# Kernel tuning notes

Hardware: AMD Instinct MI355X
Metric: run time of the kernel (lower is better)

## Reference

```python
import jax, jax.numpy as jnp
import numpy as np

DECAY = 0.99


def setup_inputs() -> dict:
    key = jax.random.key(0)
    k1, k2, k3 = jax.random.split(key, 3)
    B, D, H, W = 16, 128, 32, 32
    K = 8192
    z_e = jax.random.normal(k1, (B, D, H, W), dtype=jnp.float32)
    codebook = jax.random.normal(k2, (K, D), dtype=jnp.float32)
    ema_count = jnp.ones((K,), dtype=jnp.float32)
    ema_weight = codebook  # buffer initialized as codebook.clone()
    return {"z_e": z_e, "codebook": codebook, "ema_count": ema_count, "ema_weight": ema_weight}


def reference(z_e, codebook, ema_count, ema_weight):
    B, D, H, W = z_e.shape
    K = codebook.shape[0]
    # (B,D,H,W) -> (N,D)
    z_flat = z_e.transpose(0, 2, 3, 1).reshape(-1, D)
    # squared L2 distances: ||z||^2 - 2 z.C^T + ||C||^2  -> (N,K)
    dist = (
        jnp.sum(z_flat * z_flat, axis=1, keepdims=True)
        - 2.0 * (z_flat @ codebook.T)
        + jnp.sum(codebook * codebook, axis=1)[None, :]
    )
    indices = jnp.argmin(dist, axis=1)  # (N,)
    z_q = codebook[indices].reshape(B, H, W, D).transpose(0, 3, 1, 2)
    # EMA codebook update (training path, no grad)
    counts = jax.ops.segment_sum(jnp.ones_like(indices, dtype=jnp.float32), indices, num_segments=K)
    dw = jax.ops.segment_sum(z_flat, indices, num_segments=K)  # (K,D)
    new_count = ema_count * DECAY + (1.0 - DECAY) * counts
    new_weight = ema_weight * DECAY + (1.0 - DECAY) * dw
    new_codebook = new_weight / jnp.maximum(new_count, 1.0)[:, None]
    # straight-through estimator
    z_q_st = z_e + jax.lax.stop_gradient(z_q - z_e)
    return (z_q_st, indices.reshape(B, H, W), new_codebook, new_count, new_weight)
```

## Files before the change

### kernel.cpp

```cpp
#include <hip/hip_runtime.h>

#define D 128
#define HW 1024
#define NROWS 16384
#define K 8192
#define NU 16

#define OUT0 0
#define OUT1 2097152
#define OUT2 2113536
#define OUT3 3162112
#define OUT4 3170304

typedef __attribute__((ext_vector_type(8))) _Float16 half8;
typedef __attribute__((ext_vector_type(16))) float f32x16;
typedef unsigned short u16;
typedef unsigned long long u64;

__device__ __forceinline__ void gld16(const u16* gsrc, u16* ldst) {
    __builtin_amdgcn_global_load_lds(
        (const __attribute__((address_space(1))) unsigned int*)gsrc,
        (__attribute__((address_space(3))) unsigned int*)ldst,
        16, 0, 0);
}

__global__ __launch_bounds__(256) void k_prep_cb(const float* __restrict__ cb,
                                                 u16* __restrict__ Bg,
                                                 float* __restrict__ cnorm) {
    int tid = threadIdx.x;
    int kk = tid & 15;
    int k = blockIdx.x * 16 + (tid >> 4);
    const float* src = cb + (size_t)k * D + kk * 8;
    half8 h, l;
    float s = 0.f;
#pragma unroll
    for (int j = 0; j < 8; ++j) {
        float v = src[j];
        s += v * v;
        _Float16 hv = (_Float16)v;
        _Float16 lv = (_Float16)(v - (float)hv);
        h[j] = hv;
        l[j] = lv;
    }
    int g = k >> 7, col = k & 127;
    size_t offH = (size_t)g * 32768 + ((size_t)kk * 128 + col) * 8;
    *(half8*)((_Float16*)Bg + offH) = h;
    *(half8*)((_Float16*)Bg + offH + 16384) = l;
#pragma unroll
    for (int off = 8; off > 0; off >>= 1) s += __shfl_down(s, off);
    if (kk == 0) cnorm[k] = s;
}

__global__ __launch_bounds__(256) void k_prep_z(const float* __restrict__ z_e,
                                                u16* __restrict__ Ah, u16* __restrict__ Al) {
    int gid = blockIdx.x * 256 + threadIdx.x;
    int n  = gid & (NROWS - 1);
    int kk = gid >> 14;
    int b = n >> 10, hw = n & 1023;
    const float* src = z_e + ((size_t)b * D + kk * 8) * HW + hw;
    half8 h, l;
#pragma unroll
    for (int j = 0; j < 8; ++j) {
        float v = src[(size_t)j * HW];
        _Float16 hv = (_Float16)v;
        _Float16 lv = (_Float16)(v - (float)hv);
        h[j] = hv;
        l[j] = lv;
    }
    int rg = n >> 7, band = (n >> 5) & 3, row = n & 31;
    size_t off = (((((size_t)rg * 4 + band) * 8 + (kk >> 1)) * 2 + (kk & 1)) * 32 + row) * 8;
    *(half8*)(Ah + off) = h;
    *(half8*)(Al + off) = l;
}

__global__ __launch_bounds__(512, 2) void k_argmin_mfma(
        const u16* __restrict__ Ahg, const u16* __restrict__ Alg,
        const u16* __restrict__ Bg,
        const float* __restrict__ cnorm, u64* __restrict__ packed) {
    __shared__ u16 lds[2][32768];

    const int tid = threadIdx.x;
    const int ln  = tid & 63;
    const int l31 = ln & 31;
    const int lh  = ln >> 5;
    const int wv  = tid >> 6;
    const int wy  = wv & 3;
    const int wx  = wv >> 2;

    const int rg = blockIdx.x >> 2;
    const int k0 = (blockIdx.x & 3) * 2048;
    const int g0 = k0 >> 7;

    half8 Ah[8], Al[8];
#pragma unroll
    for (int ks = 0; ks < 8; ++ks) {
        size_t off = ((((size_t)(rg * 4 + wy) * 8 + ks) * 2 + lh) * 32 + l31) * 8;
        Ah[ks] = *(const half8*)((const _Float16*)Ahg + off);
        Al[ks] = *(const half8*)((const _Float16*)Alg + off);
    }

    {
        const u16* src = Bg + (size_t)g0 * 32768;
#pragma unroll
        for (int r = 0; r < 8; ++r)
            gld16(src + ((size_t)r * 512 + tid) * 8, lds[0] + (r * 512 + tid) * 8);
    }

    float minv[16];
    int   mini[16];
#pragma unroll
    for (int r = 0; r < 16; ++r) { minv[r] = INFINITY; mini[r] = 0; }

#pragma unroll 1
    for (int u = 0; u < NU; ++u) {
        const u16* buf = lds[u & 1];
        const int colbase = k0 + u * 128;
        const int c0 = colbase + wx * 64 + l31;

        float cn0 = cnorm[c0];
        float cn1 = cnorm[c0 + 32];

        if (u + 1 < NU) {
            const u16* src = Bg + (size_t)(g0 + u + 1) * 32768;
            u16* dst = lds[(u + 1) & 1];
#pragma unroll
            for (int r = 0; r < 8; ++r)
                gld16(src + ((size_t)r * 512 + tid) * 8, dst + (r * 512 + tid) * 8);
            asm volatile("s_waitcnt vmcnt(8)" ::: "memory");
        } else {
            asm volatile("s_waitcnt vmcnt(0)" ::: "memory");
        }
        asm volatile("s_barrier" ::: "memory");

        f32x16 acc0 = {}, acc1 = {};
        const u16* bh = buf;
        const u16* bl = buf + 16384;

#pragma unroll
        for (int ks = 0; ks < 8; ++ks) {
            const int bo = ((ks * 2 + lh) * 128 + wx * 64 + l31) * 8;
            half8 b0 = *(const half8*)((const _Float16*)bl + bo);
            half8 b1 = *(const half8*)((const _Float16*)bl + bo + 256);
            acc0 = __builtin_amdgcn_mfma_f32_32x32x16_f16(Ah[ks], b0, acc0, 0, 0, 0);
            acc1 = __builtin_amdgcn_mfma_f32_32x32x16_f16(Ah[ks], b1, acc1, 0, 0, 0);
        }
#pragma unroll
        for (int ks = 0; ks < 8; ++ks) {
            const int bo = ((ks * 2 + lh) * 128 + wx * 64 + l31) * 8;
            half8 b0 = *(const half8*)((const _Float16*)bh + bo);
            half8 b1 = *(const half8*)((const _Float16*)bh + bo + 256);
            acc0 = __builtin_amdgcn_mfma_f32_32x32x16_f16(Ah[ks], b0, acc0, 0, 0, 0);
            acc1 = __builtin_amdgcn_mfma_f32_32x32x16_f16(Ah[ks], b1, acc1, 0, 0, 0);
            acc0 = __builtin_amdgcn_mfma_f32_32x32x16_f16(Al[ks], b0, acc0, 0, 0, 0);
            acc1 = __builtin_amdgcn_mfma_f32_32x32x16_f16(Al[ks], b1, acc1, 0, 0, 0);
        }

#pragma unroll
        for (int r = 0; r < 16; ++r) {
            float d0 = fmaf(-2.0f, acc0[r], cn0);
            float d1 = fmaf(-2.0f, acc1[r], cn1);
            if (d0 < minv[r]) { minv[r] = d0; mini[r] = c0; }
            if (d1 < minv[r]) { minv[r] = d1; mini[r] = c0 + 32; }
        }
        asm volatile("s_barrier" ::: "memory");
    }

#pragma unroll
    for (int r = 0; r < 16; ++r) {
        float v = minv[r];
        int ix = mini[r];
#pragma unroll
        for (int off = 1; off < 32; off <<= 1) {
            float v2 = __shfl_xor(v, off);
            int i2 = __shfl_xor(ix, off);
            if (v2 < v || (v2 == v && i2 < ix)) { v = v2; ix = i2; }
        }
        if (l31 == 0) {
            int row = rg * 128 + wy * 32 + 4 * lh + (r & 3) + 8 * (r >> 2);
            unsigned int uenc = __float_as_uint(v);
            uenc = (uenc & 0x80000000u) ? ~uenc : (uenc | 0x80000000u);
            u64 pk = ((u64)uenc << 13) | (u64)(unsigned)ix;
            atomicMin(&packed[row], pk);
        }
    }
}

__global__ __launch_bounds__(256) void k_epilogue(const float* __restrict__ z_e,
                                                  const float* __restrict__ cb,
                                                  const u64* __restrict__ packed,
                                                  float* __restrict__ out0,
                                                  float* __restrict__ out1,
                                                  float* __restrict__ counts,
                                                  float* __restrict__ dw) {
    __shared__ int idxS[64];
    const int tid = threadIdx.x;
    const int n0 = blockIdx.x * 64;
    const int bb = n0 >> 10, p0 = n0 & 1023;

    if (tid < 64) {
        int ix = (int)(packed[n0 + tid] & 0x1FFFull);
        idxS[tid] = ix;
        out1[n0 + tid] = (float)ix;
        atomicAdd(&counts[ix], 1.0f);
    }
    __syncthreads();

    const float* zb = z_e + (size_t)bb * (D * HW) + p0;
    float* ob = out0 + (size_t)bb * (D * HW) + p0;

    for (int i = tid; i < 64 * D; i += 256) {
        int d = i >> 6, r = i & 63;
        float z = zb[(size_t)d * HW + r];
        float c = cb[(size_t)idxS[r] * D + d];
        ob[(size_t)d * HW + r] = z + (c - z);
    }
    for (int i = tid; i < 64 * D; i += 256) {
        int r = i >> 7, d = i & 127;
        atomicAdd(&dw[(size_t)idxS[r] * D + d], zb[(size_t)d * HW + r]);
    }
}

__global__ __launch_bounds__(256) void k_final(const float* __restrict__ ema_count,
                                               const float* __restrict__ ema_weight,
                                               float* __restrict__ out2,
                                               float* __restrict__ out3,
                                               float* __restrict__ out4) {
    int gid = blockIdx.x * 256 + threadIdx.x;
    int k = gid >> 7, d = gid & 127;
    float cnt_raw = out3[k];
    float dw_raw = out4[gid];
    __syncthreads();
    float nc = 0.99f * ema_count[k] + 0.01f * cnt_raw;
    float nw = 0.99f * ema_weight[gid] + 0.01f * dw_raw;
    out4[gid] = nw;
    out2[gid] = nw / fmaxf(nc, 1.0f);
    if (d == 0) out3[k] = nc;
}

extern "C" void kernel_launch(void* const* d_in, const int* in_sizes, int n_in,
                              void* d_out, int out_size, void* d_ws, size_t ws_size,
                              hipStream_t stream) {
    const float* z_e        = (const float*)d_in[0];
    const float* cb         = (const float*)d_in[1];
    const float* ema_count  = (const float*)d_in[2];
    const float* ema_weight = (const float*)d_in[3];
    float* out = (float*)d_out;

    float* cnorm = (float*)d_ws;
    u64* packed = (u64*)((char*)d_ws + K * 4);

    u16* Ahg = (u16*)(out + OUT0);
    u16* Alg = Ahg + (size_t)NROWS * D;
    u16* Bg  = (u16*)(out + OUT2);

    hipMemsetAsync(packed, 0xFF, NROWS * 8, stream);
    hipMemsetAsync(out + OUT3, 0, (size_t)(K + K * D) * 4, stream);

    k_prep_cb    <<<K / 16,           256, 0, stream>>>(cb, Bg, cnorm);
    k_prep_z     <<<NROWS * 16 / 256, 256, 0, stream>>>(z_e, Ahg, Alg);
    k_argmin_mfma<<<512,              512, 0, stream>>>(Ahg, Alg, Bg, cnorm, packed);
    k_epilogue   <<<NROWS / 64,       256, 0, stream>>>(z_e, cb, packed,
                                                        out + OUT0, out + OUT1,
                                                        out + OUT3, out + OUT4);
    k_final      <<<(K * D) / 256,    256, 0, stream>>>(ema_count, ema_weight,
                                                        out + OUT2, out + OUT3, out + OUT4);
}
```

Before: 220.8 us.

## Fuse prep kernels and memsets, halve argmin column tile for higher occupancy

Merges the codebook and z preparation kernels into one launch, which also zeroes the packed argmin buffer, counts and dw, so the two memsets go away. The argmin kernel now processes 64 codebook columns per step instead of 128, with one accumulator and a 32 KB LDS double buffer, and declares 4 blocks per CU instead of 2 to raise occupancy and latency hiding. In exchange, each step has half as many MFMAs per barrier and LDS load, and there are twice as many pipeline iterations.

New measurement: 205.6 us. 1.07x faster.

```diff
diff --git a/kernel.cpp b/kernel.cpp
--- a/kernel.cpp
+++ b/kernel.cpp
@@ -4,7 +4,7 @@
 #define HW 1024
 #define NROWS 16384
 #define K 8192
-#define NU 16
+#define NU 32
 
 #define OUT0 0
 #define OUT1 2097152
@@ -24,60 +24,72 @@
         16, 0, 0);
 }
 
-__global__ __launch_bounds__(256) void k_prep_cb(const float* __restrict__ cb,
-                                                 u16* __restrict__ Bg,
-                                                 float* __restrict__ cnorm) {
-    int tid = threadIdx.x;
-    int kk = tid & 15;
-    int k = blockIdx.x * 16 + (tid >> 4);
-    const float* src = cb + (size_t)k * D + kk * 8;
-    half8 h, l;
-    float s = 0.f;
-#pragma unroll
-    for (int j = 0; j < 8; ++j) {
-        float v = src[j];
-        s += v * v;
-        _Float16 hv = (_Float16)v;
-        _Float16 lv = (_Float16)(v - (float)hv);
-        h[j] = hv;
-        l[j] = lv;
-    }
-    int g = k >> 7, col = k & 127;
-    size_t offH = (size_t)g * 32768 + ((size_t)kk * 128 + col) * 8;
-    *(half8*)((_Float16*)Bg + offH) = h;
-    *(half8*)((_Float16*)Bg + offH + 16384) = l;
-#pragma unroll
-    for (int off = 8; off > 0; off >>= 1) s += __shfl_down(s, off);
-    if (kk == 0) cnorm[k] = s;
-}
-
-__global__ __launch_bounds__(256) void k_prep_z(const float* __restrict__ z_e,
-                                                u16* __restrict__ Ah, u16* __restrict__ Al) {
-    int gid = blockIdx.x * 256 + threadIdx.x;
-    int n  = gid & (NROWS - 1);
-    int kk = gid >> 14;
-    int b = n >> 10, hw = n & 1023;
-    const float* src = z_e + ((size_t)b * D + kk * 8) * HW + hw;
-    half8 h, l;
-#pragma unroll
-    for (int j = 0; j < 8; ++j) {
-        float v = src[(size_t)j * HW];
-        _Float16 hv = (_Float16)v;
-        _Float16 lv = (_Float16)(v - (float)hv);
-        h[j] = hv;
-        l[j] = lv;
-    }
-    int rg = n >> 7, band = (n >> 5) & 3, row = n & 31;
-    size_t off = (((((size_t)rg * 4 + band) * 8 + (kk >> 1)) * 2 + (kk & 1)) * 32 + row) * 8;
-    *(half8*)(Ah + off) = h;
-    *(half8*)(Al + off) = l;
-}
-
-__global__ __launch_bounds__(512, 2) void k_argmin_mfma(
+__global__ __launch_bounds__(256) void k_prep(const float* __restrict__ cb,
+                                              const float* __restrict__ z_e,
+                                              u16* __restrict__ Bg,
+                                              float* __restrict__ cnorm,
+                                              u16* __restrict__ Ah, u16* __restrict__ Al,
+                                              u64* __restrict__ packed,
+                                              float* __restrict__ counts,
+                                              float* __restrict__ dw) {
+    const int tid = threadIdx.x;
+    if (blockIdx.x < 512) {
+        int kk = tid & 15;
+        int k = blockIdx.x * 16 + (tid >> 4);
+        const float* src = cb + (size_t)k * D + kk * 8;
+        half8 h, l;
+        float s = 0.f;
+#pragma unroll
+        for (int j = 0; j < 8; ++j) {
+            float v = src[j];
+            s += v * v;
+            _Float16 hv = (_Float16)v;
+            _Float16 lv = (_Float16)(v - (float)hv);
+            h[j] = hv;
+            l[j] = lv;
+        }
+        int g = k >> 6, col = k & 63;
+        size_t offH = (size_t)g * 16384 + ((size_t)kk * 64 + col) * 8;
+        *(half8*)((_Float16*)Bg + offH) = h;
+        *(half8*)((_Float16*)Bg + offH + 8192) = l;
+#pragma unroll
+        for (int off = 8; off > 0; off >>= 1) s += __shfl_down(s, off);
+        if (kk == 0) cnorm[k] = s;
+        float4 z4 = {0.f, 0.f, 0.f, 0.f};
+        size_t zi = ((size_t)blockIdx.x * 256 + tid) * 8;
+        *(float4*)(dw + zi) = z4;
+        *(float4*)(dw + zi + 4) = z4;
+    } else {
+        int gid = (blockIdx.x - 512) * 256 + tid;
+        int n  = gid & (NROWS - 1);
+        int kk = gid >> 14;
+        int b = n >> 10, hw = n & 1023;
+        const float* src = z_e + ((size_t)b * D + kk * 8) * HW + hw;
+        half8 h, l;
+#pragma unroll
+        for (int j = 0; j < 8; ++j) {
+            float v = src[(size_t)j * HW];
+            _Float16 hv = (_Float16)v;
+            _Float16 lv = (_Float16)(v - (float)hv);
+            h[j] = hv;
+            l[j] = lv;
+        }
+        int rg = n >> 7, band = (n >> 5) & 3, row = n & 31;
+        size_t off = (((((size_t)rg * 4 + band) * 8 + (kk >> 1)) * 2 + (kk & 1)) * 32 + row) * 8;
+        *(half8*)(Ah + off) = h;
+        *(half8*)(Al + off) = l;
+        if (kk == 0) {
+            packed[n] = ~0ull;
+            if (n < K) counts[n] = 0.f;
+        }
+    }
+}
+
+__global__ __launch_bounds__(512, 4) void k_argmin_mfma(
         const u16* __restrict__ Ahg, const u16* __restrict__ Alg,
         const u16* __restrict__ Bg,
         const float* __restrict__ cnorm, u64* __restrict__ packed) {
-    __shared__ u16 lds[2][32768];
+    __shared__ u16 lds[2][16384];
 
     const int tid = threadIdx.x;
     const int ln  = tid & 63;
@@ -89,7 +101,7 @@
 
     const int rg = blockIdx.x >> 2;
     const int k0 = (blockIdx.x & 3) * 2048;
-    const int g0 = k0 >> 7;
+    const int g0 = k0 >> 6;
 
     half8 Ah[8], Al[8];
 #pragma unroll
@@ -100,9 +112,9 @@
     }
 
     {
-        const u16* src = Bg + (size_t)g0 * 32768;
-#pragma unroll
-        for (int r = 0; r < 8; ++r)
+        const u16* src = Bg + (size_t)g0 * 16384;
+#pragma unroll
+        for (int r = 0; r < 4; ++r)
             gld16(src + ((size_t)r * 512 + tid) * 8, lds[0] + (r * 512 + tid) * 8);
     }
 
@@ -114,53 +126,44 @@
 #pragma unroll 1
     for (int u = 0; u < NU; ++u) {
         const u16* buf = lds[u & 1];
-        const int colbase = k0 + u * 128;
-        const int c0 = colbase + wx * 64 + l31;
+        const int c0 = k0 + u * 64 + wx * 32 + l31;
 
         float cn0 = cnorm[c0];
-        float cn1 = cnorm[c0 + 32];
 
         if (u + 1 < NU) {
-            const u16* src = Bg + (size_t)(g0 + u + 1) * 32768;
+            const u16* src = Bg + (size_t)(g0 + u + 1) * 16384;
             u16* dst = lds[(u + 1) & 1];
 #pragma unroll
-            for (int r = 0; r < 8; ++r)
+            for (int r = 0; r < 4; ++r)
                 gld16(src + ((size_t)r * 512 + tid) * 8, dst + (r * 512 + tid) * 8);
-            asm volatile("s_waitcnt vmcnt(8)" ::: "memory");
+            asm volatile("s_waitcnt vmcnt(4)" ::: "memory");
         } else {
             asm volatile("s_waitcnt vmcnt(0)" ::: "memory");
         }
         asm volatile("s_barrier" ::: "memory");
 
-        f32x16 acc0 = {}, acc1 = {};
-        const u16* bh = buf;
-        const u16* bl = buf + 16384;
+        f32x16 acc = {};
+        const _Float16* bh = (const _Float16*)buf;
+        const _Float16* bl = bh + 8192;
 
 #pragma unroll
         for (int ks = 0; ks < 8; ++ks) {
-            const int bo = ((ks * 2 + lh) * 128 + wx * 64 + l31) * 8;
-            half8 b0 = *(const half8*)((const _Float16*)bl + bo);
-            half8 b1 = *(const half8*)((const _Float16*)bl + bo + 256);
-            acc0 = __builtin_amdgcn_mfma_f32_32x32x16_f16(Ah[ks], b0, acc0, 0, 0, 0);
-            acc1 = __builtin_amdgcn_mfma_f32_32x32x16_f16(Ah[ks], b1, acc1, 0, 0, 0);
+            const int bo = ((ks * 2 + lh) * 64 + wx * 32 + l31) * 8;
+            half8 b0 = *(const half8*)(bl + bo);
+            acc = __builtin_amdgcn_mfma_f32_32x32x16_f16(Ah[ks], b0, acc, 0, 0, 0);
         }
 #pragma unroll
         for (int ks = 0; ks < 8; ++ks) {
-            const int bo = ((ks * 2 + lh) * 128 + wx * 64 + l31) * 8;
-            half8 b0 = *(const half8*)((const _Float16*)bh + bo);
-            half8 b1 = *(const half8*)((const _Float16*)bh + bo + 256);
-            acc0 = __builtin_amdgcn_mfma_f32_32x32x16_f16(Ah[ks], b0, acc0, 0, 0, 0);
-            acc1 = __builtin_amdgcn_mfma_f32_32x32x16_f16(Ah[ks], b1, acc1, 0, 0, 0);
-            acc0 = __builtin_amdgcn_mfma_f32_32x32x16_f16(Al[ks], b0, acc0, 0, 0, 0);
-            acc1 = __builtin_amdgcn_mfma_f32_32x32x16_f16(Al[ks], b1, acc1, 0, 0, 0);
+            const int bo = ((ks * 2 + lh) * 64 + wx * 32 + l31) * 8;
+            half8 b0 = *(const half8*)(bh + bo);
+            acc = __builtin_amdgcn_mfma_f32_32x32x16_f16(Ah[ks], b0, acc, 0, 0, 0);
+            acc = __builtin_amdgcn_mfma_f32_32x32x16_f16(Al[ks], b0, acc, 0, 0, 0);
         }
 
 #pragma unroll
         for (int r = 0; r < 16; ++r) {
-            float d0 = fmaf(-2.0f, acc0[r], cn0);
-            float d1 = fmaf(-2.0f, acc1[r], cn1);
+            float d0 = fmaf(-2.0f, acc[r], cn0);
             if (d0 < minv[r]) { minv[r] = d0; mini[r] = c0; }
-            if (d1 < minv[r]) { minv[r] = d1; mini[r] = c0 + 32; }
         }
         asm volatile("s_barrier" ::: "memory");
     }
@@ -253,15 +256,12 @@
     u16* Alg = Ahg + (size_t)NROWS * D;
     u16* Bg  = (u16*)(out + OUT2);
 
-    hipMemsetAsync(packed, 0xFF, NROWS * 8, stream);
-    hipMemsetAsync(out + OUT3, 0, (size_t)(K + K * D) * 4, stream);
-
-    k_prep_cb    <<<K / 16,           256, 0, stream>>>(cb, Bg, cnorm);
-    k_prep_z     <<<NROWS * 16 / 256, 256, 0, stream>>>(z_e, Ahg, Alg);
-    k_argmin_mfma<<<512,              512, 0, stream>>>(Ahg, Alg, Bg, cnorm, packed);
-    k_epilogue   <<<NROWS / 64,       256, 0, stream>>>(z_e, cb, packed,
-                                                        out + OUT0, out + OUT1,
-                                                        out + OUT3, out + OUT4);
-    k_final      <<<(K * D) / 256,    256, 0, stream>>>(ema_count, ema_weight,
-                                                        out + OUT2, out + OUT3, out + OUT4);
-}
+    k_prep       <<<1536,          256, 0, stream>>>(cb, z_e, Bg, cnorm, Ahg, Alg,
+                                                     packed, out + OUT3, out + OUT4);
+    k_argmin_mfma<<<512,           512, 0, stream>>>(Ahg, Alg, Bg, cnorm, packed);
+    k_epilogue   <<<NROWS / 64,    256, 0, stream>>>(z_e, cb, packed,
+                                                     out + OUT0, out + OUT1,
+                                                     out + OUT3, out + OUT4);
+    k_final      <<<(K * D) / 256, 256, 0, stream>>>(ema_count, ema_weight,
+                                                     out + OUT2, out + OUT3, out + OUT4);
+}
```
